# Performance work log

Hardware: AMD Instinct MI355X
Metric: run time of the kernel (lower is better)

Reference implementation:

```python
import jax, jax.numpy as jnp
import numpy as np
from jax import lax


def setup_inputs() -> dict:
    key = jax.random.key(0)
    ks = jax.random.split(key, 8)
    B, N, q = 16, 4096, 256
    sc = float(1.0 / np.sqrt(q))
    return {
        "u": jax.random.normal(ks[0], (B, N, q), jnp.float32),
        "a": jax.random.normal(ks[1], (q,), jnp.float32),  # diag of A
        "W_B": jax.random.normal(ks[2], (q, q), jnp.float32) * sc,
        "b_B": jax.random.normal(ks[3], (q,), jnp.float32) * sc,
        "W_C": jax.random.normal(ks[4], (q, q), jnp.float32) * sc,
        "b_C": jax.random.normal(ks[5], (q,), jnp.float32) * sc,
        "W_D": jax.random.normal(ks[6], (q, q), jnp.float32) * sc,
        "b_D": jax.random.normal(ks[7], (q,), jnp.float32) * sc,
    }


def _solve_im(u, a, W_B, b_B, dt):
    """IM solver. A is diagonal, so M_inv is four diagonal blocks:
    new_x = s*x - dt*s*a*z ; new_z = dt*s*x + s*z, with s = 1/(1+dt^2*a).
    Forcing F = M_inv @ [dt*B(u); 0] -> (dt*s*Bu, dt^2*s*Bu)."""
    s = 1.0 / (1.0 + dt * dt * a)  # (q,)
    Bu = jnp.einsum("bnq,pq->bnp", u, W_B) + b_B  # (B,N,q), torch Linear: u @ W^T + b
    f_x = (dt * s) * Bu
    f_z = (dt * dt * s) * Bu
    dsa = dt * s * a
    ds = dt * s

    def step(carry, f):
        x, z = carry
        fx, fz = f
        x_new = s * x - dsa * z + fx
        z_new = ds * x + s * z + fz
        return (x_new, z_new), z_new

    Bsz, _, q = u.shape
    init = (jnp.zeros((Bsz, q), u.dtype), jnp.zeros((Bsz, q), u.dtype))
    # scan over time axis
    _, z_t = lax.scan(step, init, (jnp.moveaxis(f_x, 1, 0), jnp.moveaxis(f_z, 1, 0)))
    return jnp.moveaxis(z_t, 0, 1)  # (B,N,q) -- the out[..., size:] half


def reference(u, a, W_B, b_B, W_C, b_C, W_D, b_D):
    N = u.shape[1]
    dt = 1.0 / N
    y = _solve_im(u, a, W_B, b_B, dt)
    x = (jnp.einsum("bnq,pq->bnp", y, W_C) + b_C) + (jnp.einsum("bnq,pq->bnp", u, W_D) + b_D)
    x = jax.nn.gelu(x, approximate=False)  # torch GELU default = exact erf
    # GLU(concat([x, x], -1)) == x * sigmoid(x)
    out = x * jax.nn.sigmoid(x) + u
    return (out, y)
```

## Files before the change

kernel.cpp:

```cpp
#include <hip/hip_runtime.h>
#include <hip/hip_bf16.h>
#include <cstdint>

typedef __bf16 bf16_t;
typedef __bf16 bf16x8 __attribute__((ext_vector_type(8)));
typedef float f32x4 __attribute__((ext_vector_type(4)));

#define B_SZ 16
#define N_SZ 4096
#define Q_SZ 256
#define M_TOT (B_SZ * N_SZ)
#define DT (1.0f / 4096.0f)
#define LDST 40
#define CHUNKS 64
#define LOG2_CLEN 6
#define CLEN (N_SZ / CHUNKS)
#define PF 8


__device__ __forceinline__ bf16x8 load8f(const float* p) {
  const float4 v0 = *(const float4*)p;
  const float4 v1 = *(const float4*)(p + 4);
  bf16x8 v;
  v[0] = (bf16_t)v0.x; v[1] = (bf16_t)v0.y; v[2] = (bf16_t)v0.z; v[3] = (bf16_t)v0.w;
  v[4] = (bf16_t)v1.x; v[5] = (bf16_t)v1.y; v[6] = (bf16_t)v1.z; v[7] = (bf16_t)v1.w;
  return v;
}

__device__ __forceinline__ int pidx(int tm, int tk, int lane) {
  return ((tm * 8 + tk) * 64 + lane) * 8;
}

__device__ __forceinline__ void kpassP(const bf16_t* __restrict__ A,
                                       const bf16_t* __restrict__ Bw,
                                       int tmA, int tnB, int lane,
                                       f32x4 acc[4][4]) {
#pragma unroll
  for (int tk = 0; tk < 8; ++tk) {
    bf16x8 af[4], bv[4];
#pragma unroll
    for (int i = 0; i < 4; ++i) {
      af[i] = *(const bf16x8*)(A + pidx(tmA + i, tk, lane));
      bv[i] = *(const bf16x8*)(Bw + pidx(tnB + i, tk, lane));
    }
#pragma unroll
    for (int mi = 0; mi < 4; ++mi)
#pragma unroll
      for (int ni = 0; ni < 4; ++ni)
        acc[mi][ni] = __builtin_amdgcn_mfma_f32_16x16x32_bf16(af[mi], bv[ni],
                                                              acc[mi][ni], 0, 0, 0);
  }
}

__global__ __launch_bounds__(256) void prep_kernel(
    const float* __restrict__ u, const float* __restrict__ WB,
    const float* __restrict__ WC, const float* __restrict__ WD,
    bf16_t* __restrict__ ubP, bf16_t* __restrict__ WBbP,
    bf16_t* __restrict__ WCbP, bf16_t* __restrict__ WDbP) {
  const int g = blockIdx.x * 256 + threadIdx.x;
  const int UC = (M_TOT * Q_SZ) / 8;
  const float* src;
  bf16_t* dst;
  int cidx;
  if (g < UC) {
    src = u; dst = ubP; cidx = g;
  } else {
    const int h = g - UC;
    const int w = h >> 13;
    cidx = h & 8191;
    src = (w == 0) ? WB : (w == 1) ? WC : WD;
    dst = (w == 0) ? WBbP : (w == 1) ? WCbP : WDbP;
  }
  const int lane = cidx & 63, tk = (cidx >> 6) & 7, tm = cidx >> 9;
  const int row = tm * 16 + (lane & 15);
  const int col = tk * 32 + (lane >> 4) * 8;
  *(bf16x8*)(dst + (size_t)cidx * 8) = load8f(src + (size_t)row * Q_SZ + col);
}

__global__ __launch_bounds__(256, 2) void gemm1f_kernel(
    const bf16_t* __restrict__ ubP, const bf16_t* __restrict__ WBbP,
    const float* __restrict__ a, const float* __restrict__ bB,
    float* __restrict__ ex, float* __restrict__ ez,
    float* __restrict__ lzP) {
  __shared__ float T[2][64][128];
  const int t = threadIdx.x;
  const int bid = blockIdx.x;
  const int swz = (bid & 7) * 128 + (bid >> 3);
  const int m0 = (swz >> 1) * 128, n0 = (swz & 1) * 128;
  const int lane = t & 63, ln = lane & 15, quad = lane >> 4;
  const int wave = t >> 6;
  const int wm = (wave & 1) * 64, wn = (wave >> 1) * 64;
  f32x4 acc[4][4] = {};
  kpassP(ubP, WBbP, (m0 + wm) >> 4, (n0 + wn) >> 4, lane, acc);

  const int cc = wave & 1;
#pragma unroll
  for (int ni = 0; ni < 4; ++ni) {
    const int colL = wn + ni * 16 + ln;
    const int gp = n0 + colL;
    const float av = a[gp];
    const float s = 1.0f / (1.0f + DT * DT * av);
    const float sc = DT * s;
    const float bb = bB[gp];
#pragma unroll
    for (int mi = 0; mi < 4; ++mi) {
      const int nrow = mi * 16 + quad * 4;
#pragma unroll
      for (int r2 = 0; r2 < 4; ++r2)
        T[cc][nrow + r2][colL] = sc * (acc[mi][ni][r2] + bb);
    }
  }
  __syncthreads();

  const int scc = t >> 7, col = t & 127;
  const int pg = n0 + col;
  {
    const float av = a[pg];
    const float s = 1.0f / (1.0f + DT * DT * av);
    const float dsa = DT * s * av, dss = DT * s;
    const int mbase = m0 + scc * 64;
    const int tkp = pg >> 5, e = pg & 7;
    const int plane = (((pg >> 3) & 3) << 4);
    float x = 0.f, z = 0.f;
#pragma unroll 8
    for (int n = 0; n < 64; ++n) {
      const float f = T[scc][n][col];
      const float xn = fmaf(s, x, fmaf(-dsa, z, f));
      const float zn = fmaf(dss, x, fmaf(s, z, DT * f));
      x = xn; z = zn;
      const int m = mbase + n;
      const int tm = m >> 4;
      lzP[(size_t)(((tm * 8 + tkp) * 64 + (plane | (m & 15)))) * 8 + e] = zn;
    }
    const int chunk_g = mbase >> 6;
    ex[chunk_g * 256 + pg] = x;
    ez[chunk_g * 256 + pg] = z;
  }
}

__global__ __launch_bounds__(256) void scan2_kernel(
    const float* __restrict__ a, const float* __restrict__ ex,
    const float* __restrict__ ez, float* __restrict__ ix, float* __restrict__ iz) {
  const int g = blockIdx.x * 256 + threadIdx.x;
  const int p = g & 255, b = g >> 8;
  const float av = a[p];
  const float s = 1.0f / (1.0f + DT * DT * av);
  float m00 = s, m01 = -DT * s * av, m10 = DT * s, m11 = s;
#pragma unroll
  for (int i = 0; i < LOG2_CLEN; ++i) {
    const float a00 = fmaf(m00, m00, m01 * m10);
    const float a01 = m01 * (m00 + m11);
    const float a10 = m10 * (m00 + m11);
    const float a11 = fmaf(m11, m11, m01 * m10);
    m00 = a00; m01 = a01; m10 = a10; m11 = a11;
  }
  float x = 0.f, z = 0.f;
  for (int c = 0; c < CHUNKS; ++c) {
    const size_t idx = ((size_t)b * CHUNKS + c) * Q_SZ + p;
    ix[idx] = x; iz[idx] = z;
    const float xn = fmaf(m00, x, fmaf(m01, z, ex[idx]));
    const float zn = fmaf(m10, x, fmaf(m11, z, ez[idx]));
    x = xn; z = zn;
  }
}

__global__ __launch_bounds__(256) void mpow_kernel(
    const float* __restrict__ a, float* __restrict__ t10,
    float* __restrict__ t11) {
  const int p = threadIdx.x;
  const float av = a[p];
  const float s = 1.0f / (1.0f + DT * DT * av);
  const float m00 = s, m01 = -DT * s * av, m10 = DT * s, m11 = s;
  float p00 = m00, p01 = m01, p10 = m10, p11 = m11;
  for (int n = 0; n < 64; ++n) {
    t10[n * 256 + p] = p10;
    t11[n * 256 + p] = p11;
    const float q00 = fmaf(m00, p00, m01 * p10);
    const float q01 = fmaf(m00, p01, m01 * p11);
    const float q10 = fmaf(m10, p00, m11 * p10);
    const float q11 = fmaf(m10, p01, m11 * p11);
    p00 = q00; p01 = q01; p10 = q10; p11 = q11;
  }
}

__global__ __launch_bounds__(256, 2) void gemm2f_kernel(
    const float* __restrict__ lzP, const bf16_t* __restrict__ WCbP,
    const bf16_t* __restrict__ ubP, const bf16_t* __restrict__ WDbP,
    const float* __restrict__ ix, const float* __restrict__ iz,
    const float* __restrict__ t10, const float* __restrict__ t11,
    const float* __restrict__ u, const float* __restrict__ bC,
    const float* __restrict__ bD, float* __restrict__ yout,
    float* __restrict__ out0) {
  const int t = threadIdx.x;
  const int bid = blockIdx.x;
  const int swz = (bid & 7) * 128 + (bid >> 3);
  const int m0 = (swz >> 1) * 128, n0 = (swz & 1) * 128;
  const int lane = t & 63, ln = lane & 15, quad = lane >> 4;
  const int wave = t >> 6;
  const int wm = (wave & 1) * 64, wn = (wave >> 1) * 64;
  const int tmA = (m0 + wm) >> 4, tnB = (n0 + wn) >> 4;
  const bool wY = (n0 == 0) && (wn == 0);
  f32x4 acc[4][4] = {};
#pragma unroll
  for (int tk = 0; tk < 8; ++tk) {
    bf16x8 af[4], bv[4], a2[4], b2[4];
#pragma unroll
    for (int i = 0; i < 4; ++i) {
      const float* lp = lzP + (size_t)(((tmA + i) * 8 + tk) * 64 + lane) * 8;
      const f32x4 l0 = *(const f32x4*)lp;
      const f32x4 l1 = *(const f32x4*)(lp + 4);
      const int m = (tmA + i) * 16 + ln;
      const int nloc = m & 63, cg = m >> 6;
      const int p0 = tk * 32 + quad * 8;
      const f32x4 tA0 = *(const f32x4*)(t10 + nloc * 256 + p0);
      const f32x4 tA1 = *(const f32x4*)(t10 + nloc * 256 + p0 + 4);
      const f32x4 tB0 = *(const f32x4*)(t11 + nloc * 256 + p0);
      const f32x4 tB1 = *(const f32x4*)(t11 + nloc * 256 + p0 + 4);
      const f32x4 X0 = *(const f32x4*)(ix + cg * 256 + p0);
      const f32x4 X1 = *(const f32x4*)(ix + cg * 256 + p0 + 4);
      const f32x4 Z0 = *(const f32x4*)(iz + cg * 256 + p0);
      const f32x4 Z1 = *(const f32x4*)(iz + cg * 256 + p0 + 4);
      f32x4 y0, y1;
#pragma unroll
      for (int e = 0; e < 4; ++e) {
        y0[e] = fmaf(tA0[e], X0[e], fmaf(tB0[e], Z0[e], l0[e]));
        y1[e] = fmaf(tA1[e], X1[e], fmaf(tB1[e], Z1[e], l1[e]));
      }
      if (wY) {
        *(f32x4*)(yout + (size_t)m * Q_SZ + p0) = y0;
        *(f32x4*)(yout + (size_t)m * Q_SZ + p0 + 4) = y1;
      }
      bf16x8 av_;
#pragma unroll
      for (int e = 0; e < 4; ++e) {
        av_[e] = (bf16_t)y0[e];
        av_[e + 4] = (bf16_t)y1[e];
      }
      af[i] = av_;
      a2[i] = *(const bf16x8*)(ubP + pidx(tmA + i, tk, lane));
      bv[i] = *(const bf16x8*)(WCbP + pidx(tnB + i, tk, lane));
      b2[i] = *(const bf16x8*)(WDbP + pidx(tnB + i, tk, lane));
    }
#pragma unroll
    for (int mi = 0; mi < 4; ++mi)
#pragma unroll
      for (int ni = 0; ni < 4; ++ni)
        acc[mi][ni] = __builtin_amdgcn_mfma_f32_16x16x32_bf16(af[mi], bv[ni],
                                                              acc[mi][ni], 0, 0, 0);
#pragma unroll
    for (int mi = 0; mi < 4; ++mi)
#pragma unroll
      for (int ni = 0; ni < 4; ++ni)
        acc[mi][ni] = __builtin_amdgcn_mfma_f32_16x16x32_bf16(a2[mi], b2[ni],
                                                              acc[mi][ni], 0, 0, 0);
  }
#pragma unroll
  for (int ni = 0; ni < 4; ++ni) {
    const int gp = n0 + wn + ni * 16 + ln;
    const float bias = bC[gp] + bD[gp];
#pragma unroll
    for (int mi = 0; mi < 4; ++mi) {
      const int gm = m0 + wm + mi * 16 + quad * 4;
#pragma unroll
      for (int r2 = 0; r2 < 4; ++r2) {
        const float x = acc[mi][ni][r2] + bias;
        const float g = 0.5f * x * (1.0f + erff(x * 0.70710678118654752f));
        const float sg = 1.0f / (1.0f + __expf(-g));
        const float uu = u[(size_t)(gm + r2) * Q_SZ + gp];
        out0[(size_t)(gm + r2) * Q_SZ + gp] = fmaf(g, sg, uu);
      }
    }
  }
}


__device__ __forceinline__ void kloop(const float* __restrict__ Ap,
                                      const float* __restrict__ Bp,
                                      int m0, int n0, int t,
                                      bf16_t* As, bf16_t* Bs, f32x4 acc[4][4]) {
  const int r = t >> 2, cc = t & 3;
  const int lane = t & 63, ln = lane & 15, quad = lane >> 4;
  const int wave = t >> 6;
  const int wm = (wave & 1) * 64, wn = (wave >> 1) * 64;

  for (int k0 = 0; k0 < Q_SZ; k0 += 32) {
#pragma unroll
    for (int i = 0; i < 2; ++i) {
      const int row = r + i * 64;
      const int col = k0 + cc * 8;
      *(bf16x8*)(As + row * LDST + cc * 8) =
          load8f(Ap + (size_t)(m0 + row) * Q_SZ + col);
      *(bf16x8*)(Bs + row * LDST + cc * 8) =
          load8f(Bp + (size_t)(n0 + row) * Q_SZ + col);
    }
    __syncthreads();
    bf16x8 af[4], bv[4];
#pragma unroll
    for (int mi = 0; mi < 4; ++mi) {
      af[mi] = *(const bf16x8*)(As + (wm + mi * 16 + ln) * LDST + quad * 8);
      bv[mi] = *(const bf16x8*)(Bs + (wn + mi * 16 + ln) * LDST + quad * 8);
    }
#pragma unroll
    for (int mi = 0; mi < 4; ++mi)
#pragma unroll
      for (int ni = 0; ni < 4; ++ni)
        acc[mi][ni] = __builtin_amdgcn_mfma_f32_16x16x32_bf16(af[mi], bv[ni],
                                                              acc[mi][ni], 0, 0, 0);
    __syncthreads();
  }
}

__global__ __launch_bounds__(256) void gemm1_kernel(
    const float* __restrict__ u, const float* __restrict__ WB,
    const float* __restrict__ a, const float* __restrict__ bB,
    float* __restrict__ fx) {
  __shared__ __align__(16) bf16_t As[128 * LDST];
  __shared__ __align__(16) bf16_t Bs[128 * LDST];
  const int t = threadIdx.x;
  const int m0 = blockIdx.x * 128, n0 = blockIdx.y * 128;
  f32x4 acc[4][4] = {};
  kloop(u, WB, m0, n0, t, As, Bs, acc);

  const int lane = t & 63, ln = lane & 15, quad = lane >> 4;
  const int wave = t >> 6;
  const int wm = (wave & 1) * 64, wn = (wave >> 1) * 64;
#pragma unroll
  for (int ni = 0; ni < 4; ++ni) {
    const int gp = n0 + wn + ni * 16 + ln;
    const float av = a[gp];
    const float s = 1.0f / (1.0f + DT * DT * av);
    const float sc = DT * s;
    const float bb = bB[gp];
#pragma unroll
    for (int mi = 0; mi < 4; ++mi) {
      const int gm = m0 + wm + mi * 16 + quad * 4;
#pragma unroll
      for (int r2 = 0; r2 < 4; ++r2)
        fx[(size_t)(gm + r2) * Q_SZ + gp] = sc * (acc[mi][ni][r2] + bb);
    }
  }
}

__global__ __launch_bounds__(256) void gemm2_kernel(
    const float* __restrict__ y, const float* __restrict__ WC,
    const float* __restrict__ u, const float* __restrict__ WD,
    const float* __restrict__ bC, const float* __restrict__ bD,
    float* __restrict__ out0) {
  __shared__ __align__(16) bf16_t As[128 * LDST];
  __shared__ __align__(16) bf16_t Bs[128 * LDST];
  const int t = threadIdx.x;
  const int m0 = blockIdx.x * 128, n0 = blockIdx.y * 128;
  f32x4 acc[4][4] = {};
  kloop(y, WC, m0, n0, t, As, Bs, acc);
  kloop(u, WD, m0, n0, t, As, Bs, acc);

  const int lane = t & 63, ln = lane & 15, quad = lane >> 4;
  const int wave = t >> 6;
  const int wm = (wave & 1) * 64, wn = (wave >> 1) * 64;
#pragma unroll
  for (int ni = 0; ni < 4; ++ni) {
    const int gp = n0 + wn + ni * 16 + ln;
    const float bias = bC[gp] + bD[gp];
#pragma unroll
    for (int mi = 0; mi < 4; ++mi) {
      const int gm = m0 + wm + mi * 16 + quad * 4;
#pragma unroll
      for (int r2 = 0; r2 < 4; ++r2) {
        const float x = acc[mi][ni][r2] + bias;
        const float g = 0.5f * x * (1.0f + erff(x * 0.70710678118654752f));
        const float sg = 1.0f / (1.0f + __expf(-g));
        const float uu = u[(size_t)(gm + r2) * Q_SZ + gp];
        out0[(size_t)(gm + r2) * Q_SZ + gp] = fmaf(g, sg, uu);
      }
    }
  }
}

__global__ __launch_bounds__(256) void scan1_kernel(
    const float* __restrict__ fx, const float* __restrict__ a,
    float* __restrict__ ex, float* __restrict__ ez) {
  const int g = blockIdx.x * 256 + threadIdx.x;
  const int p = g & 255, c = (g >> 8) & (CHUNKS - 1), b = g >> 14;
  const float av = a[p];
  const float s = 1.0f / (1.0f + DT * DT * av);
  const float dsa = DT * s * av, dss = DT * s;
  float x = 0.f, z = 0.f;
  const float* fp = fx + ((size_t)b * N_SZ + c * CLEN) * Q_SZ + p;
  for (int n = 0; n < CLEN; ++n) {
    const float f = fp[(size_t)n * Q_SZ];
    const float xn = fmaf(s, x, fmaf(-dsa, z, f));
    const float zn = fmaf(dss, x, fmaf(s, z, DT * f));
    x = xn; z = zn;
  }
  ex[g] = x; ez[g] = z;
}

__global__ __launch_bounds__(256) void scan3_kernel(
    const float* __restrict__ a, const float* __restrict__ ix,
    const float* __restrict__ iz, float* __restrict__ yf) {
  const int g = blockIdx.x * 256 + threadIdx.x;
  const int p = g & 255, c = (g >> 8) & (CHUNKS - 1), b = g >> 14;
  const float av = a[p];
  const float s = 1.0f / (1.0f + DT * DT * av);
  const float dsa = DT * s * av, dss = DT * s;
  float x = ix[g], z = iz[g];
  float* yp = yf + ((size_t)b * N_SZ + c * CLEN) * Q_SZ + p;
  for (int n = 0; n < CLEN; ++n) {
    const float f = yp[(size_t)n * Q_SZ];
    const float xn = fmaf(s, x, fmaf(-dsa, z, f));
    const float zn = fmaf(dss, x, fmaf(s, z, DT * f));
    x = xn; z = zn;
    yp[(size_t)n * Q_SZ] = zn;
  }
}

__global__ __launch_bounds__(256) void scan_mono_kernel(
    const float* __restrict__ a, float* __restrict__ yf) {
  const int g = blockIdx.x * 256 + threadIdx.x;
  const int p = g & 255, b = g >> 8;
  const float av = a[p];
  const float s = 1.0f / (1.0f + DT * DT * av);
  const float dsa = DT * s * av, dss = DT * s;
  float x = 0.f, z = 0.f;
  float* yp = yf + (size_t)b * N_SZ * Q_SZ + p;
  for (int n = 0; n < N_SZ; ++n) {
    const float f = yp[(size_t)n * Q_SZ];
    const float xn = fmaf(s, x, fmaf(-dsa, z, f));
    const float zn = fmaf(dss, x, fmaf(s, z, DT * f));
    x = xn; z = zn;
    yp[(size_t)n * Q_SZ] = zn;
  }
}


extern "C" void kernel_launch(void* const* d_in, const int* in_sizes, int n_in,
                              void* d_out, int out_size, void* d_ws, size_t ws_size,
                              hipStream_t stream) {
  const float* u  = (const float*)d_in[0];
  const float* a  = (const float*)d_in[1];
  const float* WB = (const float*)d_in[2];
  const float* bB = (const float*)d_in[3];
  const float* WC = (const float*)d_in[4];
  const float* bC = (const float*)d_in[5];
  const float* WD = (const float*)d_in[6];
  const float* bD = (const float*)d_in[7];

  float* out0 = (float*)d_out;
  float* yreg = out0 + (size_t)M_TOT * Q_SZ;

  const size_t UB_ELEMS = (size_t)M_TOT * Q_SZ;
  const size_t W_ELEMS = (size_t)Q_SZ * Q_SZ;
  const size_t ST_ELEMS = (size_t)B_SZ * CHUNKS * Q_SZ;
  const size_t need_full =
      UB_ELEMS * sizeof(bf16_t) + 3 * W_ELEMS * sizeof(bf16_t) +
      UB_ELEMS * sizeof(float) + 4 * ST_ELEMS * sizeof(float) +
      2 * 64 * 256 * sizeof(float);
  const size_t state_bytes = 4 * ST_ELEMS * sizeof(float);

  if (ws_size >= need_full) {
    bf16_t* ubP  = (bf16_t*)d_ws;
    bf16_t* WBbP = ubP + UB_ELEMS;
    bf16_t* WCbP = WBbP + W_ELEMS;
    bf16_t* WDbP = WCbP + W_ELEMS;
    float* lzP = (float*)(WDbP + W_ELEMS);
    float* ex = lzP + UB_ELEMS;
    float* ez = ex + ST_ELEMS;
    float* ix = ez + ST_ELEMS;
    float* iz = ix + ST_ELEMS;
    float* t10 = iz + ST_ELEMS;
    float* t11 = t10 + 64 * 256;

    prep_kernel<<<8288, 256, 0, stream>>>(u, WB, WC, WD, ubP, WBbP, WCbP, WDbP);
    gemm1f_kernel<<<1024, 256, 0, stream>>>(ubP, WBbP, a, bB, ex, ez, lzP);
    scan2_kernel<<<16, 256, 0, stream>>>(a, ex, ez, ix, iz);
    mpow_kernel<<<1, 256, 0, stream>>>(a, t10, t11);
    gemm2f_kernel<<<1024, 256, 0, stream>>>(lzP, WCbP, ubP, WDbP, ix, iz,
                                            t10, t11, u, bC, bD, yreg, out0);
  } else {
    dim3 gg(M_TOT / 128, Q_SZ / 128);
    gemm1_kernel<<<gg, 256, 0, stream>>>(u, WB, a, bB, yreg);
    if (ws_size >= state_bytes) {
      float* ex = (float*)d_ws;
      float* ez = ex + ST_ELEMS;
      float* ix = ez + ST_ELEMS;
      float* iz = ix + ST_ELEMS;
      scan1_kernel<<<1024, 256, 0, stream>>>(yreg, a, ex, ez);
      scan2_kernel<<<16, 256, 0, stream>>>(a, ex, ez, ix, iz);
      scan3_kernel<<<1024, 256, 0, stream>>>(a, ix, iz, yreg);
    } else {
      scan_mono_kernel<<<16, 256, 0, stream>>>(a, yreg);
    }
    gemm2_kernel<<<gg, 256, 0, stream>>>(yreg, WC, u, WD, bC, bD, out0);
  }
}
```

Measured before the change: 395.0 us.

## Split chunk-state fixup into separate kernel emitting packed bf16 y for GEMM2

gemm1f now writes local scan results directly into the row-major y output instead of a packed fp32 scratch buffer. A new fix3 kernel applies the chunk-carry correction in place on y and writes a bf16 MFMA-packed copy of y. gemm2 then only loads bf16 operands, no longer doing redundant fixup work across both column blocks. The shared staging array is also padded to 133 columns to reduce LDS bank conflicts. The cost is an extra kernel launch plus an extra read/write pass over y, in exchange for a leaner GEMM inner loop and half-size A operand traffic.

```diff
diff --git a/kernel.cpp b/kernel.cpp
--- a/kernel.cpp
+++ b/kernel.cpp
@@ -15,7 +15,7 @@
 #define CHUNKS 64
 #define LOG2_CLEN 6
 #define CLEN (N_SZ / CHUNKS)
-#define PF 8
+#define TPAD 133
 
 
 __device__ __forceinline__ bf16x8 load8f(const float* p) {
@@ -81,8 +81,8 @@
     const bf16_t* __restrict__ ubP, const bf16_t* __restrict__ WBbP,
     const float* __restrict__ a, const float* __restrict__ bB,
     float* __restrict__ ex, float* __restrict__ ez,
-    float* __restrict__ lzP) {
-  __shared__ float T[2][64][128];
+    float* __restrict__ lz) {
+  __shared__ float T[2][64][TPAD];
   const int t = threadIdx.x;
   const int bid = blockIdx.x;
   const int swz = (bid & 7) * 128 + (bid >> 3);
@@ -119,18 +119,15 @@
     const float s = 1.0f / (1.0f + DT * DT * av);
     const float dsa = DT * s * av, dss = DT * s;
     const int mbase = m0 + scc * 64;
-    const int tkp = pg >> 5, e = pg & 7;
-    const int plane = (((pg >> 3) & 3) << 4);
     float x = 0.f, z = 0.f;
+    float* lp = lz + (size_t)mbase * Q_SZ + pg;
 #pragma unroll 8
     for (int n = 0; n < 64; ++n) {
       const float f = T[scc][n][col];
       const float xn = fmaf(s, x, fmaf(-dsa, z, f));
       const float zn = fmaf(dss, x, fmaf(s, z, DT * f));
       x = xn; z = zn;
-      const int m = mbase + n;
-      const int tm = m >> 4;
-      lzP[(size_t)(((tm * 8 + tkp) * 64 + (plane | (m & 15)))) * 8 + e] = zn;
+      lp[(size_t)n * Q_SZ] = zn;
     }
     const int chunk_g = mbase >> 6;
     ex[chunk_g * 256 + pg] = x;
@@ -183,14 +180,48 @@
   }
 }
 
-__global__ __launch_bounds__(256, 2) void gemm2f_kernel(
-    const float* __restrict__ lzP, const bf16_t* __restrict__ WCbP,
-    const bf16_t* __restrict__ ubP, const bf16_t* __restrict__ WDbP,
+__global__ __launch_bounds__(256) void fix3_kernel(
     const float* __restrict__ ix, const float* __restrict__ iz,
     const float* __restrict__ t10, const float* __restrict__ t11,
+    float* __restrict__ y, bf16_t* __restrict__ ybP) {
+  const int g = blockIdx.x * 256 + threadIdx.x;
+  const int m = g >> 5, p0 = (g & 31) * 8;
+  const int nloc = m & 63, cg = m >> 6;
+  float* yp = y + (size_t)m * Q_SZ + p0;
+  const f32x4 l0 = *(const f32x4*)yp;
+  const f32x4 l1 = *(const f32x4*)(yp + 4);
+  const f32x4 tA0 = *(const f32x4*)(t10 + nloc * 256 + p0);
+  const f32x4 tA1 = *(const f32x4*)(t10 + nloc * 256 + p0 + 4);
+  const f32x4 tB0 = *(const f32x4*)(t11 + nloc * 256 + p0);
+  const f32x4 tB1 = *(const f32x4*)(t11 + nloc * 256 + p0 + 4);
+  const f32x4 X0 = *(const f32x4*)(ix + cg * 256 + p0);
+  const f32x4 X1 = *(const f32x4*)(ix + cg * 256 + p0 + 4);
+  const f32x4 Z0 = *(const f32x4*)(iz + cg * 256 + p0);
+  const f32x4 Z1 = *(const f32x4*)(iz + cg * 256 + p0 + 4);
+  f32x4 y0, y1;
+#pragma unroll
+  for (int e = 0; e < 4; ++e) {
+    y0[e] = fmaf(tA0[e], X0[e], fmaf(tB0[e], Z0[e], l0[e]));
+    y1[e] = fmaf(tA1[e], X1[e], fmaf(tB1[e], Z1[e], l1[e]));
+  }
+  *(f32x4*)yp = y0;
+  *(f32x4*)(yp + 4) = y1;
+  bf16x8 v;
+#pragma unroll
+  for (int e = 0; e < 4; ++e) {
+    v[e] = (bf16_t)y0[e];
+    v[e + 4] = (bf16_t)y1[e];
+  }
+  const int chunk = ((m >> 4) * 8 + (p0 >> 5)) * 64 +
+                    ((((p0 >> 3) & 3) << 4) | (m & 15));
+  *(bf16x8*)(ybP + (size_t)chunk * 8) = v;
+}
+
+__global__ __launch_bounds__(256, 2) void gemm2p_kernel(
+    const bf16_t* __restrict__ ybP, const bf16_t* __restrict__ WCbP,
+    const bf16_t* __restrict__ ubP, const bf16_t* __restrict__ WDbP,
     const float* __restrict__ u, const float* __restrict__ bC,
-    const float* __restrict__ bD, float* __restrict__ yout,
-    float* __restrict__ out0) {
+    const float* __restrict__ bD, float* __restrict__ out0) {
   const int t = threadIdx.x;
   const int bid = blockIdx.x;
   const int swz = (bid & 7) * 128 + (bid >> 3);
@@ -199,53 +230,22 @@
   const int wave = t >> 6;
   const int wm = (wave & 1) * 64, wn = (wave >> 1) * 64;
   const int tmA = (m0 + wm) >> 4, tnB = (n0 + wn) >> 4;
-  const bool wY = (n0 == 0) && (wn == 0);
   f32x4 acc[4][4] = {};
 #pragma unroll
   for (int tk = 0; tk < 8; ++tk) {
-    bf16x8 af[4], bv[4], a2[4], b2[4];
+    bf16x8 a1[4], b1[4], a2[4], b2[4];
 #pragma unroll
     for (int i = 0; i < 4; ++i) {
-      const float* lp = lzP + (size_t)(((tmA + i) * 8 + tk) * 64 + lane) * 8;
-      const f32x4 l0 = *(const f32x4*)lp;
-      const f32x4 l1 = *(const f32x4*)(lp + 4);
-      const int m = (tmA + i) * 16 + ln;
-      const int nloc = m & 63, cg = m >> 6;
-      const int p0 = tk * 32 + quad * 8;
-      const f32x4 tA0 = *(const f32x4*)(t10 + nloc * 256 + p0);
-      const f32x4 tA1 = *(const f32x4*)(t10 + nloc * 256 + p0 + 4);
-      const f32x4 tB0 = *(const f32x4*)(t11 + nloc * 256 + p0);
-      const f32x4 tB1 = *(const f32x4*)(t11 + nloc * 256 + p0 + 4);
-      const f32x4 X0 = *(const f32x4*)(ix + cg * 256 + p0);
-      const f32x4 X1 = *(const f32x4*)(ix + cg * 256 + p0 + 4);
-      const f32x4 Z0 = *(const f32x4*)(iz + cg * 256 + p0);
-      const f32x4 Z1 = *(const f32x4*)(iz + cg * 256 + p0 + 4);
-      f32x4 y0, y1;
-#pragma unroll
-      for (int e = 0; e < 4; ++e) {
-        y0[e] = fmaf(tA0[e], X0[e], fmaf(tB0[e], Z0[e], l0[e]));
-        y1[e] = fmaf(tA1[e], X1[e], fmaf(tB1[e], Z1[e], l1[e]));
-      }
-      if (wY) {
-        *(f32x4*)(yout + (size_t)m * Q_SZ + p0) = y0;
-        *(f32x4*)(yout + (size_t)m * Q_SZ + p0 + 4) = y1;
-      }
-      bf16x8 av_;
-#pragma unroll
-      for (int e = 0; e < 4; ++e) {
-        av_[e] = (bf16_t)y0[e];
-        av_[e + 4] = (bf16_t)y1[e];
-      }
-      af[i] = av_;
+      a1[i] = *(const bf16x8*)(ybP + pidx(tmA + i, tk, lane));
+      b1[i] = *(const bf16x8*)(WCbP + pidx(tnB + i, tk, lane));
       a2[i] = *(const bf16x8*)(ubP + pidx(tmA + i, tk, lane));
-      bv[i] = *(const bf16x8*)(WCbP + pidx(tnB + i, tk, lane));
       b2[i] = *(const bf16x8*)(WDbP + pidx(tnB + i, tk, lane));
     }
 #pragma unroll
     for (int mi = 0; mi < 4; ++mi)
 #pragma unroll
       for (int ni = 0; ni < 4; ++ni)
-        acc[mi][ni] = __builtin_amdgcn_mfma_f32_16x16x32_bf16(af[mi], bv[ni],
+        acc[mi][ni] = __builtin_amdgcn_mfma_f32_16x16x32_bf16(a1[mi], b1[ni],
                                                               acc[mi][ni], 0, 0, 0);
 #pragma unroll
     for (int mi = 0; mi < 4; ++mi)
@@ -452,18 +452,20 @@
   const size_t W_ELEMS = (size_t)Q_SZ * Q_SZ;
   const size_t ST_ELEMS = (size_t)B_SZ * CHUNKS * Q_SZ;
   const size_t need_full =
-      UB_ELEMS * sizeof(bf16_t) + 3 * W_ELEMS * sizeof(bf16_t) +
-      UB_ELEMS * sizeof(float) + 4 * ST_ELEMS * sizeof(float) +
+      UB_ELEMS * sizeof(bf16_t) +
+      UB_ELEMS * sizeof(bf16_t) +
+      3 * W_ELEMS * sizeof(bf16_t) +
+      4 * ST_ELEMS * sizeof(float) +
       2 * 64 * 256 * sizeof(float);
   const size_t state_bytes = 4 * ST_ELEMS * sizeof(float);
 
   if (ws_size >= need_full) {
     bf16_t* ubP  = (bf16_t*)d_ws;
-    bf16_t* WBbP = ubP + UB_ELEMS;
+    bf16_t* ybP  = ubP + UB_ELEMS;
+    bf16_t* WBbP = ybP + UB_ELEMS;
     bf16_t* WCbP = WBbP + W_ELEMS;
     bf16_t* WDbP = WCbP + W_ELEMS;
-    float* lzP = (float*)(WDbP + W_ELEMS);
-    float* ex = lzP + UB_ELEMS;
+    float* ex = (float*)(WDbP + W_ELEMS);
     float* ez = ex + ST_ELEMS;
     float* ix = ez + ST_ELEMS;
     float* iz = ix + ST_ELEMS;
@@ -471,11 +473,11 @@
     float* t11 = t10 + 64 * 256;
 
     prep_kernel<<<8288, 256, 0, stream>>>(u, WB, WC, WD, ubP, WBbP, WCbP, WDbP);
-    gemm1f_kernel<<<1024, 256, 0, stream>>>(ubP, WBbP, a, bB, ex, ez, lzP);
+    gemm1f_kernel<<<1024, 256, 0, stream>>>(ubP, WBbP, a, bB, ex, ez, yreg);
     scan2_kernel<<<16, 256, 0, stream>>>(a, ex, ez, ix, iz);
     mpow_kernel<<<1, 256, 0, stream>>>(a, t10, t11);
-    gemm2f_kernel<<<1024, 256, 0, stream>>>(lzP, WCbP, ubP, WDbP, ix, iz,
-                                            t10, t11, u, bC, bD, yreg, out0);
+    fix3_kernel<<<8192, 256, 0, stream>>>(ix, iz, t10, t11, yreg, ybP);
+    gemm2p_kernel<<<1024, 256, 0, stream>>>(ybP, WCbP, ubP, WDbP, u, bC, bD, out0);
   } else {
     dim3 gg(M_TOT / 128, Q_SZ / 128);
     gemm1_kernel<<<gg, 256, 0, stream>>>(u, WB, a, bB, yreg);
```

Result: faster. 325.0 us (-17.7%).
